# Kernel tuning notes

Measured on AMD Instinct MI355X. Metric: run time of the kernel, lower is better.

## Reference

```python
import jax, jax.numpy as jnp
import numpy as np

OUTPUT_DIM = 2000
INPUT_DIM = 8192
N_COLS = 2000  # must equal OUTPUT_DIM so bias broadcasts over last dim as in the torch code
SPARSITY = 0.9
BLOCK = 4


def _apply_block_sparsity(weight, block=BLOCK, sparsity=SPARSITY, seed=1234):
    # Zero out 4x4 blocks with probability `sparsity`, mirroring apply_block_sparsity.
    rng = np.random.RandomState(seed)
    rb = (weight.shape[0] + block - 1) // block
    cb = (weight.shape[1] + block - 1) // block
    keep = (rng.rand(rb, cb) <= (1.0 - sparsity)).astype(np.float32)
    mask = np.kron(keep, np.ones((block, block), dtype=np.float32))
    return weight * mask[: weight.shape[0], : weight.shape[1]]


def setup_inputs() -> dict:
    key = jax.random.key(0)
    k_w, k_b, k_x = jax.random.split(key, 3)
    weight = np.asarray(jax.random.normal(k_w, (OUTPUT_DIM, INPUT_DIM), dtype=jnp.float32))
    weight = jnp.asarray(_apply_block_sparsity(weight))
    bias = jax.random.normal(k_b, (OUTPUT_DIM,), dtype=jnp.float32)
    x = jax.random.normal(k_x, (INPUT_DIM, N_COLS), dtype=jnp.float32)
    return {"weight": weight, "bias": bias, "x": x}


def reference(weight, bias, x):
    # [OUT, IN] @ [IN, N] -> [OUT, N]; bias [OUT] broadcasts over last dim (N == OUT here),
    # exactly matching torch.matmul(weight, x) + bias.
    return jnp.matmul(weight, x) + bias
```

## Files before the change

### kernel.cpp

```cpp
#include <hip/hip_runtime.h>

#define K_DIM 8192
#define M_REAL 2000
#define N_REAL 2000
#define M_PAD 2048
#define N_PAD 2048

#define BM 256
#define BN 256
#define BK 32
#define SPLITK 4
#define KSLAB (K_DIM / SPLITK)
#define NIT (KSLAB / BK)

#define NB_CONVW 16384
#define NB_CONVX 4096
#define NB_INIT  3907

typedef __bf16 bf16x8 __attribute__((ext_vector_type(8)));
typedef float f32x4 __attribute__((ext_vector_type(4)));
typedef float fvec4 __attribute__((ext_vector_type(4)));

#define RAW_BARRIER()  asm volatile("s_barrier" ::: "memory")
#define WAIT_VM4()     asm volatile("s_waitcnt vmcnt(4)" ::: "memory")
#define WAIT_VM0()     asm volatile("s_waitcnt vmcnt(0)" ::: "memory")

__device__ __forceinline__ unsigned short f2bf(float f) {
    union { float f; unsigned u; } v; v.f = f;
    unsigned r = v.u + 0x7FFFu + ((v.u >> 16) & 1u);
    return (unsigned short)(r >> 16);
}

__device__ __forceinline__ void async16(const void* g, void* l) {
    __builtin_amdgcn_global_load_lds((__attribute__((address_space(1))) void*)(g),
                                     (__attribute__((address_space(3))) void*)(l),
                                     16, 0, 0);
}

__global__ __launch_bounds__(256) void prep_kernel(const float* __restrict__ W,
                                                   const float* __restrict__ X,
                                                   const float* __restrict__ bias,
                                                   unsigned short* __restrict__ Wb,
                                                   unsigned short* __restrict__ XT,
                                                   float* __restrict__ out) {
    __shared__ unsigned short tile[64][68];
    int bid = blockIdx.x;
    if (bid < NB_CONVW) {
        long long t = (long long)bid * 256 + threadIdx.x;
        long long e = t * 4;
        int m = (int)(e >> 13);
        ushort4 o = make_ushort4(0, 0, 0, 0);
        if (m < M_REAL) {
            fvec4 f = __builtin_nontemporal_load((const fvec4*)(W + e));
            o.x = f2bf(f.x); o.y = f2bf(f.y); o.z = f2bf(f.z); o.w = f2bf(f.w);
        }
        *(ushort4*)(Wb + e) = o;
    } else if (bid < NB_CONVW + NB_CONVX) {
        int b2 = bid - NB_CONVW;
        int k0 = (b2 & 127) * 64;
        int n0 = (b2 >> 7) * 64;
        int t = threadIdx.x;
        int c16 = t & 15, r16 = t >> 4;
#pragma unroll
        for (int it = 0; it < 4; ++it) {
            int k = k0 + r16 + it * 16;
            int n = n0 + c16 * 4;
            fvec4 v = {0.f, 0.f, 0.f, 0.f};
            if (n < N_REAL)
                v = __builtin_nontemporal_load((const fvec4*)(X + (long long)k * N_REAL + n));
            ushort4 o;
            o.x = f2bf(v.x); o.y = f2bf(v.y); o.z = f2bf(v.z); o.w = f2bf(v.w);
            *(ushort4*)&tile[r16 + it * 16][c16 * 4] = o;
        }
        __syncthreads();
#pragma unroll
        for (int it = 0; it < 4; ++it) {
            int nn = r16 + it * 16;
            int k4 = c16 * 4;
            ushort4 o;
            o.x = tile[k4 + 0][nn];
            o.y = tile[k4 + 1][nn];
            o.z = tile[k4 + 2][nn];
            o.w = tile[k4 + 3][nn];
            *(ushort4*)(XT + (long long)(n0 + nn) * K_DIM + k0 + k4) = o;
        }
    } else {
        int t = (bid - NB_CONVW - NB_CONVX) * 256 + threadIdx.x;
        if (t < M_REAL * (N_REAL / 4)) {
            int m = t / (N_REAL / 4);
            int n4 = t - m * (N_REAL / 4);
            float4 bv = *(const float4*)(bias + n4 * 4);
            *(float4*)(out + (long long)m * N_REAL + n4 * 4) = bv;
        }
    }
}

__global__ __launch_bounds__(512, 2) void gemm_kernel(const unsigned short* __restrict__ Wb,
                                                      const unsigned short* __restrict__ XT,
                                                      float* __restrict__ out) {
    __shared__ __align__(16) unsigned short As[2][BM * BK];
    __shared__ __align__(16) unsigned short Bs[2][BN * BK];

    int f = blockIdx.x;
    int xcd = f & 7;
    int local = f >> 3;
    int bz = local & 3;
    int bx = (xcd & 3) * 2 + ((local >> 2) & 1);
    int by = (xcd >> 2) * 4 + (local >> 3);

    int t = threadIdx.x;
    int w = t >> 6;
    int l = t & 63;
    int wm = (w >> 2) * 128;
    int wn = (w & 3) * 64;
    int lane16 = l & 15;
    int quad = l >> 4;
    int m0 = by * BM;
    int n0 = bx * BN;
    int ks = bz * KSLAB;

    f32x4 acc[8][4] = {};

    int srow = l >> 2;
    int scol = (l & 3) * 8;
    int rb = w * 32;
    const unsigned short* gA0 = Wb + (long long)(m0 + rb + srow) * K_DIM + ks + scol;
    const unsigned short* gA1 = gA0 + 16LL * K_DIM;
    const unsigned short* gB0 = XT + (long long)(n0 + rb + srow) * K_DIM + ks + scol;
    const unsigned short* gB1 = gB0 + 16LL * K_DIM;

    async16(gA0, &As[0][rb * BK]);
    async16(gA1, &As[0][(rb + 16) * BK]);
    async16(gB0, &Bs[0][rb * BK]);
    async16(gB1, &Bs[0][(rb + 16) * BK]);
    gA0 += BK; gA1 += BK; gB0 += BK; gB1 += BK;

    for (int kt = 0; kt < NIT; ++kt) {
        int cur = kt & 1;
        if (kt + 1 < NIT) {
            int nxt = cur ^ 1;
            async16(gA0, &As[nxt][rb * BK]);
            async16(gA1, &As[nxt][(rb + 16) * BK]);
            async16(gB0, &Bs[nxt][rb * BK]);
            async16(gB1, &Bs[nxt][(rb + 16) * BK]);
            gA0 += BK; gA1 += BK; gB0 += BK; gB1 += BK;
            WAIT_VM4();
        } else {
            WAIT_VM0();
        }
        RAW_BARRIER();

        bf16x8 a[8], b[4];
#pragma unroll
        for (int i = 0; i < 8; ++i)
            a[i] = *(const bf16x8*)&As[cur][(wm + i * 16 + lane16) * BK + quad * 8];
#pragma unroll
        for (int j = 0; j < 4; ++j)
            b[j] = *(const bf16x8*)&Bs[cur][(wn + j * 16 + lane16) * BK + quad * 8];

#pragma unroll
        for (int i = 0; i < 8; ++i)
#pragma unroll
            for (int j = 0; j < 4; ++j)
                acc[i][j] = __builtin_amdgcn_mfma_f32_16x16x32_bf16(a[i], b[j], acc[i][j], 0, 0, 0);

        if (kt + 1 < NIT)
            RAW_BARRIER();
    }

#pragma unroll
    for (int j = 0; j < 4; ++j) {
        int n = n0 + wn + j * 16 + lane16;
        if (n >= N_REAL) continue;
#pragma unroll
        for (int i = 0; i < 8; ++i) {
            int mbase = m0 + wm + i * 16 + quad * 4;
#pragma unroll
            for (int r = 0; r < 4; ++r) {
                int m = mbase + r;
                if (m < M_REAL)
                    atomicAdd(&out[(long long)m * N_REAL + n], acc[i][j][r]);
            }
        }
    }
}

extern "C" void kernel_launch(void* const* d_in, const int* in_sizes, int n_in,
                              void* d_out, int out_size, void* d_ws, size_t ws_size,
                              hipStream_t stream) {
    const float* W    = (const float*)d_in[0];
    const float* bias = (const float*)d_in[1];
    const float* X    = (const float*)d_in[2];
    float* out = (float*)d_out;

    unsigned short* Wb = (unsigned short*)d_ws;
    unsigned short* XT = Wb + (long long)M_PAD * K_DIM;

    prep_kernel<<<NB_CONVW + NB_CONVX + NB_INIT, 256, 0, stream>>>(W, X, bias, Wb, XT, out);

    gemm_kernel<<<(N_PAD / BN) * (M_PAD / BM) * SPLITK, 512, 0, stream>>>(Wb, XT, out);
}
```

Measured before the change: 267.1 us.

## Split prep into separate W-convert, X-transpose, and bias-init kernels with wider accesses

Replaces the single fused prep kernel with three kernels. W conversion now uses 8 elements per thread per iteration, with grid-stride loops and 16-byte stores. The X transpose covers 128x64 tiles with packed bf16 pairs and 16-byte stores to XT. Bias init uses a grid-stride loop over 1024 blocks. The intent is fewer, wider memory transactions and less per-block launch overhead in the bandwidth-bound conversion stage, at the cost of two extra kernel launches and lost overlap between the branches.

```diff
diff --git a/kernel.cpp b/kernel.cpp
--- a/kernel.cpp
+++ b/kernel.cpp
@@ -13,10 +13,6 @@
 #define KSLAB (K_DIM / SPLITK)
 #define NIT (KSLAB / BK)
 
-#define NB_CONVW 16384
-#define NB_CONVX 4096
-#define NB_INIT  3907
-
 typedef __bf16 bf16x8 __attribute__((ext_vector_type(8)));
 typedef float f32x4 __attribute__((ext_vector_type(4)));
 typedef float fvec4 __attribute__((ext_vector_type(4)));
@@ -31,67 +27,81 @@
     return (unsigned short)(r >> 16);
 }
 
+__device__ __forceinline__ unsigned pk2(float a, float b) {
+    return (unsigned)f2bf(a) | ((unsigned)f2bf(b) << 16);
+}
+
 __device__ __forceinline__ void async16(const void* g, void* l) {
     __builtin_amdgcn_global_load_lds((__attribute__((address_space(1))) void*)(g),
                                      (__attribute__((address_space(3))) void*)(l),
                                      16, 0, 0);
 }
 
-__global__ __launch_bounds__(256) void prep_kernel(const float* __restrict__ W,
-                                                   const float* __restrict__ X,
-                                                   const float* __restrict__ bias,
-                                                   unsigned short* __restrict__ Wb,
-                                                   unsigned short* __restrict__ XT,
-                                                   float* __restrict__ out) {
-    __shared__ unsigned short tile[64][68];
-    int bid = blockIdx.x;
-    if (bid < NB_CONVW) {
-        long long t = (long long)bid * 256 + threadIdx.x;
-        long long e = t * 4;
-        int m = (int)(e >> 13);
-        ushort4 o = make_ushort4(0, 0, 0, 0);
-        if (m < M_REAL) {
-            fvec4 f = __builtin_nontemporal_load((const fvec4*)(W + e));
-            o.x = f2bf(f.x); o.y = f2bf(f.y); o.z = f2bf(f.z); o.w = f2bf(f.w);
-        }
-        *(ushort4*)(Wb + e) = o;
-    } else if (bid < NB_CONVW + NB_CONVX) {
-        int b2 = bid - NB_CONVW;
-        int k0 = (b2 & 127) * 64;
-        int n0 = (b2 >> 7) * 64;
-        int t = threadIdx.x;
-        int c16 = t & 15, r16 = t >> 4;
-#pragma unroll
-        for (int it = 0; it < 4; ++it) {
-            int k = k0 + r16 + it * 16;
-            int n = n0 + c16 * 4;
-            fvec4 v = {0.f, 0.f, 0.f, 0.f};
-            if (n < N_REAL)
-                v = __builtin_nontemporal_load((const fvec4*)(X + (long long)k * N_REAL + n));
-            ushort4 o;
-            o.x = f2bf(v.x); o.y = f2bf(v.y); o.z = f2bf(v.z); o.w = f2bf(v.w);
-            *(ushort4*)&tile[r16 + it * 16][c16 * 4] = o;
-        }
-        __syncthreads();
-#pragma unroll
-        for (int it = 0; it < 4; ++it) {
-            int nn = r16 + it * 16;
-            int k4 = c16 * 4;
-            ushort4 o;
-            o.x = tile[k4 + 0][nn];
-            o.y = tile[k4 + 1][nn];
-            o.z = tile[k4 + 2][nn];
-            o.w = tile[k4 + 3][nn];
-            *(ushort4*)(XT + (long long)(n0 + nn) * K_DIM + k0 + k4) = o;
-        }
-    } else {
-        int t = (bid - NB_CONVW - NB_CONVX) * 256 + threadIdx.x;
-        if (t < M_REAL * (N_REAL / 4)) {
-            int m = t / (N_REAL / 4);
-            int n4 = t - m * (N_REAL / 4);
-            float4 bv = *(const float4*)(bias + n4 * 4);
-            *(float4*)(out + (long long)m * N_REAL + n4 * 4) = bv;
-        }
+__global__ __launch_bounds__(256) void prep_w(const float* __restrict__ W,
+                                              unsigned short* __restrict__ Wb) {
+    unsigned tid = blockIdx.x * 256u + threadIdx.x;
+#pragma unroll
+    for (unsigned i = 0; i < 8; ++i) {
+        unsigned e = (i * (1024u * 256u) + tid) * 8u;
+        uint4 o = make_uint4(0u, 0u, 0u, 0u);
+        if (e < (unsigned)(M_REAL * K_DIM)) {
+            fvec4 f0 = __builtin_nontemporal_load((const fvec4*)(W + e));
+            fvec4 f1 = __builtin_nontemporal_load((const fvec4*)(W + e + 4));
+            o.x = pk2(f0.x, f0.y);
+            o.y = pk2(f0.z, f0.w);
+            o.z = pk2(f1.x, f1.y);
+            o.w = pk2(f1.z, f1.w);
+        }
+        *(uint4*)(Wb + e) = o;
+    }
+}
+
+__global__ __launch_bounds__(256) void prep_x(const float* __restrict__ X,
+                                              unsigned short* __restrict__ XT) {
+    __shared__ unsigned short T[64][130];
+    int b = blockIdx.x;
+    int k0 = (b & 63) << 7;
+    int n0 = (b >> 6) << 6;
+    int t = threadIdx.x;
+    int c = t & 15;
+    int r = t >> 4;
+    int nl = c << 2;
+    int n = n0 + nl;
+    bool valid = (n < N_REAL);
+#pragma unroll
+    for (int p = 0; p < 4; ++p) {
+        int kl = (r << 1) + (p << 5);
+        fvec4 v0 = {0.f, 0.f, 0.f, 0.f};
+        fvec4 v1 = {0.f, 0.f, 0.f, 0.f};
+        if (valid) {
+            v0 = __builtin_nontemporal_load((const fvec4*)(X + (k0 + kl) * N_REAL + n));
+            v1 = __builtin_nontemporal_load((const fvec4*)(X + (k0 + kl + 1) * N_REAL + n));
+        }
+        *(unsigned*)&T[nl + 0][kl] = pk2(v0.x, v1.x);
+        *(unsigned*)&T[nl + 1][kl] = pk2(v0.y, v1.y);
+        *(unsigned*)&T[nl + 2][kl] = pk2(v0.z, v1.z);
+        *(unsigned*)&T[nl + 3][kl] = pk2(v0.w, v1.w);
+    }
+    __syncthreads();
+#pragma unroll
+    for (int it = 0; it < 4; ++it) {
+        int nl2 = r + (it << 4);
+        int kl2 = c << 3;
+        const unsigned* tp = (const unsigned*)&T[nl2][kl2];
+        uint4 o;
+        o.x = tp[0]; o.y = tp[1]; o.z = tp[2]; o.w = tp[3];
+        *(uint4*)(XT + (((n0 + nl2) << 13) + k0 + kl2)) = o;
+    }
+}
+
+__global__ __launch_bounds__(256) void prep_init(const float* __restrict__ bias,
+                                                 float* __restrict__ out) {
+    const int total = M_REAL * (N_REAL / 4);
+    for (int i = blockIdx.x * 256 + threadIdx.x; i < total; i += 1024 * 256) {
+        int m = i / (N_REAL / 4);
+        int n4 = i - m * (N_REAL / 4);
+        float4 bv = *(const float4*)(bias + (n4 << 2));
+        *(float4*)(out + m * N_REAL + (n4 << 2)) = bv;
     }
 }
 
@@ -196,7 +206,9 @@
     unsigned short* Wb = (unsigned short*)d_ws;
     unsigned short* XT = Wb + (long long)M_PAD * K_DIM;
 
-    prep_kernel<<<NB_CONVW + NB_CONVX + NB_INIT, 256, 0, stream>>>(W, X, bias, Wb, XT, out);
+    prep_w<<<1024, 256, 0, stream>>>(W, Wb);
+    prep_x<<<2048, 256, 0, stream>>>(X, XT);
+    prep_init<<<1024, 256, 0, stream>>>(bias, out);
 
     gemm_kernel<<<(N_PAD / BN) * (M_PAD / BM) * SPLITK, 512, 0, stream>>>(Wb, XT, out);
 }
```

Result: no change. 270.0 us (+1.1%).
